# Kernel tuning notes

Hardware: AMD Instinct MI355X
Metric: run time of the kernel (lower is better)

Reference implementation:

```python
import jax, jax.numpy as jnp
import numpy as np

NUM_CH = 4
N_NODES = 20000
N_EDGES = 320000
HEADS = 4
HID = 32
NEG_SLOPE = 0.2


def _edge_type_meta(num_ch):
    # order: spatial (ch->ch) then inter-channel (src!=dst), matching __init__
    src_t = list(range(num_ch)) + [s for s in range(num_ch) for d in range(num_ch) if s != d]
    dst_t = list(range(num_ch)) + [d for s in range(num_ch) for d in range(num_ch) if s != d]
    return src_t, dst_t


def gat_conv(x_src, x_dst, edge_index, W, a_src, a_dst, b):
    """PyG GATConv, concat=False, add_self_loops=False. x_src:[Ns,Fin], W:[Fin,H*C]."""
    H, C = a_src.shape
    n_dst = x_dst.shape[0]
    h_src = (x_src @ W).reshape(-1, H, C)           # [Ns,H,C]
    h_dst = (x_dst @ W).reshape(-1, H, C)           # [Nd,H,C] (shared lin)
    s_score = jnp.sum(h_src * a_src, axis=-1)       # [Ns,H]
    d_score = jnp.sum(h_dst * a_dst, axis=-1)       # [Nd,H]
    src, dst = edge_index[0], edge_index[1]
    e = jax.nn.leaky_relu(s_score[src] + d_score[dst], NEG_SLOPE)  # [E,H]
    # segment softmax over incoming edges of each destination node
    emax = jnp.full((n_dst, H), -jnp.inf, e.dtype).at[dst].max(e)
    p = jnp.exp(e - emax[dst])
    denom = jnp.zeros((n_dst, H), e.dtype).at[dst].add(p)
    alpha = p / denom[dst]                          # [E,H]
    msg = h_src[src] * alpha[:, :, None]            # [E,H,C]
    out = jnp.zeros((n_dst, H, C), msg.dtype).at[dst].add(msg)
    return out.mean(axis=1) + b                     # concat=False -> head mean, + bias


def hetero_layer(x_list, edges, src_t, dst_t, W, a_s, a_d, b):
    num_ch = len(x_list)
    sums = [None] * num_ch
    counts = [0] * num_ch
    for t in range(edges.shape[0]):
        o = gat_conv(x_list[src_t[t]], x_list[dst_t[t]], edges[t], W[t], a_s[t], a_d[t], b[t])
        c = dst_t[t]
        sums[c] = o if sums[c] is None else sums[c] + o
        counts[c] += 1
    return [s / cnt for s, cnt in zip(sums, counts)]  # HeteroConv aggr='mean'


def setup_inputs() -> dict:
    key = jax.random.key(0)
    ks = jax.random.split(key, 10)
    T = NUM_CH + NUM_CH * (NUM_CH - 1)
    scale = 0.1
    return {
        "x": jax.random.normal(ks[0], (NUM_CH, N_NODES, 1), jnp.float32),
        "edges": jax.random.randint(ks[1], (T, 2, N_EDGES), 0, N_NODES, jnp.int32),
        "W1": scale * jax.random.normal(ks[2], (T, 1, HEADS * HID), jnp.float32),
        "att_src1": scale * jax.random.normal(ks[3], (T, HEADS, HID), jnp.float32),
        "att_dst1": scale * jax.random.normal(ks[4], (T, HEADS, HID), jnp.float32),
        "b1": scale * jax.random.normal(ks[5], (T, HID), jnp.float32),
        "W2": scale * jax.random.normal(ks[6], (T, HID, HEADS * HID), jnp.float32),
        "att_src2": scale * jax.random.normal(ks[7], (T, HEADS, HID), jnp.float32),
        "att_dst2": scale * jax.random.normal(ks[8], (T, HEADS, HID), jnp.float32),
        "b2": scale * jax.random.normal(ks[9], (T, HID), jnp.float32),
    }


def reference(x, edges, W1, att_src1, att_dst1, b1, W2, att_src2, att_dst2, b2):
    num_ch = x.shape[0]
    src_t, dst_t = _edge_type_meta(num_ch)
    x_list = [x[c] for c in range(num_ch)]
    h = hetero_layer(x_list, edges, src_t, dst_t, W1, att_src1, att_dst1, b1)
    h = [jax.nn.relu(v) for v in h]  # dropout is identity at inference
    h = hetero_layer(h, edges, src_t, dst_t, W2, att_src2, att_dst2, b2)
    h = [jax.nn.relu(v) for v in h]
    # cat over sorted node-type keys 'ch_0'..'ch_{C-1}' (string sort == numeric for C<=10)
    return jnp.concatenate(h, axis=-1)  # [N, num_ch*HID]
```

## Files before the change

kernel.cpp:

```cpp
#include <hip/hip_runtime.h>
#include <hip/hip_fp16.h>
#include <math.h>

#define NN 20000
#define NE 320000
#define NT 16
#define NEG 0.2f
#define NCHUNK 16
#define CHSZ (NE / NCHUNK)
#define CAP 48

__device__ __forceinline__ int d_src_of(int t) { return t < 4 ? t : (t - 4) / 3; }
__device__ __forceinline__ int d_dst_of(int t) {
    if (t < 4) return t;
    int i = t - 4, s = i / 3, j = i % 3;
    return j + (j >= s ? 1 : 0);
}

__global__ __launch_bounds__(1024) void place3(const int* __restrict__ edges,
                                               unsigned* __restrict__ gcnt,
                                               unsigned short* __restrict__ csr_src) {
    int t = blockIdx.x & 15, chunk = blockIdx.x >> 4;
    __shared__ unsigned h[NN / 2];
    __shared__ unsigned base[NN / 2];
    for (int i = threadIdx.x; i < NN / 2; i += 1024) h[i] = 0;
    __syncthreads();
    const int* srcp = edges + (size_t)t * 2 * NE + chunk * CHSZ;
    const int* dstp = srcp + NE;
    for (int e = threadIdx.x; e < CHSZ; e += 1024) {
        int d = __builtin_nontemporal_load(dstp + e);
        atomicAdd(&h[d >> 1], (d & 1) ? 0x10000u : 1u);
    }
    __syncthreads();
    unsigned* gc = gcnt + (size_t)t * (NN / 2);
    for (int w = threadIdx.x; w < NN / 2; w += 1024) {
        unsigned v = h[w];
        base[w] = v ? atomicAdd(&gc[w], v) : 0u;
        h[w] = 0;
    }
    __syncthreads();
    unsigned short* cs = csr_src + (size_t)t * NN * CAP;
    for (int e = threadIdx.x; e < CHSZ; e += 1024) {
        int d = __builtin_nontemporal_load(dstp + e);
        int sv = __builtin_nontemporal_load(srcp + e);
        unsigned old = atomicAdd(&h[d >> 1], (d & 1) ? 0x10000u : 1u);
        unsigned bs = base[d >> 1];
        int off = (d & 1) ? (int)((old >> 16) + (bs >> 16))
                          : (int)((old & 0xffffu) + (bs & 0xffffu));
        if (off < CAP) cs[(size_t)d * CAP + off] = (unsigned short)sv;
    }
}

__global__ void precompute_u(const float* __restrict__ W1, const float* __restrict__ as1,
                             const float* __restrict__ ad1, const float* __restrict__ W2,
                             const float* __restrict__ as2, const float* __restrict__ ad2,
                             float* __restrict__ u1s, float* __restrict__ u1d,
                             float* __restrict__ u2s, float* __restrict__ u2d) {
    int t = blockIdx.x, tid = threadIdx.x;
    int k = tid >> 2, h = tid & 3;
    float ss = 0.f, dd = 0.f;
    for (int c = 0; c < 32; c++) {
        float w = W2[(size_t)t * 4096 + k * 128 + h * 32 + c];
        ss += w * as2[t * 128 + h * 32 + c];
        dd += w * ad2[t * 128 + h * 32 + c];
    }
    u2s[(t * 32 + k) * 4 + h] = ss;
    u2d[(t * 32 + k) * 4 + h] = dd;
    if (tid < 4) {
        int hh = tid;
        float s1 = 0.f, d1 = 0.f;
        for (int c = 0; c < 32; c++) {
            float w = W1[t * 128 + hh * 32 + c];
            s1 += w * as1[t * 128 + hh * 32 + c];
            d1 += w * ad1[t * 128 + hh * 32 + c];
        }
        u1s[t * 4 + hh] = s1;
        u1d[t * 4 + hh] = d1;
    }
}

__global__ void layer1_fused(const float* __restrict__ x, const unsigned short* __restrict__ csr_src,
                             const unsigned short* __restrict__ cnt16, const float* __restrict__ u1s,
                             const float* __restrict__ u1d, float4* __restrict__ g1) {
    int t = blockIdx.y;
    int d = blockIdx.x * 256 + threadIdx.x;
    if (d >= NN) return;
    int sc = d_src_of(t), dc = d_dst_of(t);
    float xd = x[dc * NN + d];
    float4 usv = ((const float4*)u1s)[t];
    float4 udv = ((const float4*)u1d)[t];
    float us[4] = {usv.x, usv.y, usv.z, usv.w};
    float dl[4] = {xd * udv.x, xd * udv.y, xd * udv.z, xd * udv.w};
    int cnt = cnt16[t * NN + d];
    if (cnt > CAP) cnt = CAP;
    float dn[4] = {0, 0, 0, 0}, a[4] = {0, 0, 0, 0};
    const unsigned short* cs = csr_src + (size_t)t * NN * CAP + (size_t)d * CAP;
#pragma unroll 2
    for (int i = 0; i < cnt; i++) {
        int s = cs[i];
        float xs = x[sc * NN + s];
#pragma unroll
        for (int h = 0; h < 4; h++) {
            float l = xs * us[h] + dl[h];
            l = l > 0.f ? l : NEG * l;
            float p = __expf(l);
            dn[h] += p;
            a[h] += p * xs;
        }
    }
    float4 g;
    g.x = (cnt > 0) ? a[0] / dn[0] : 0.f;
    g.y = (cnt > 0) ? a[1] / dn[1] : 0.f;
    g.z = (cnt > 0) ? a[2] / dn[2] : 0.f;
    g.w = (cnt > 0) ? a[3] / dn[3] : 0.f;
    g1[t * NN + d] = g;
}

__global__ void transform1(const float4* __restrict__ g1, const float* __restrict__ W1,
                           const float* __restrict__ b1, float* __restrict__ x1,
                           __half* __restrict__ x1h) {
    int idx = blockIdx.x * 256 + threadIdx.x;
    if (idx >= 4 * NN * 32) return;
    int c = idx & 31;
    int n = (idx >> 5) % NN;
    int ch = idx / (NN * 32);
    float sum = 0.f, bs = 0.f;
#pragma unroll
    for (int t = 0; t < NT; t++) {
        if (d_dst_of(t) == ch) {
            float4 g = g1[t * NN + n];
            const float* w = W1 + t * 128 + c;
            sum += 0.25f * (g.x * w[0] + g.y * w[32] + g.z * w[64] + g.w * w[96]);
            bs += b1[t * 32 + c];
        }
    }
    float v = 0.25f * (sum + bs);
    v = v > 0.f ? v : 0.f;
    x1[idx] = v;
    x1h[idx] = __float2half(v);
}

__global__ void scores2b(const float* __restrict__ x1, const float* __restrict__ u2s,
                         const float* __restrict__ u2d, float4* __restrict__ ss,
                         float4* __restrict__ ds) {
    int c = blockIdx.y >> 1, half = blockIdx.y & 1;
    int t0 = c, t1, t2, t3;
    if (half == 0) {
        t1 = 4 + c * 3; t2 = t1 + 1; t3 = t1 + 2;
    } else {
        int s1 = (c == 0) ? 1 : 0, s2 = (c <= 1) ? 2 : 1, s3 = (c <= 2) ? 3 : 2;
        t1 = 4 + s1 * 3 + (c > s1 ? c - 1 : c);
        t2 = 4 + s2 * 3 + (c > s2 ? c - 1 : c);
        t3 = 4 + s3 * 3 + (c > s3 ? c - 1 : c);
    }
    __shared__ float4 uS[4][32];
    const float* ub = half ? u2d : u2s;
    if (threadIdx.x < 128) {
        int q = threadIdx.x >> 5, kk = threadIdx.x & 31;
        int tq = (q == 0) ? t0 : (q == 1) ? t1 : (q == 2) ? t2 : t3;
        uS[q][kk] = ((const float4*)(ub + (size_t)tq * 128))[kk];
    }
    __syncthreads();
    int n = blockIdx.x * 256 + threadIdx.x;
    if (n >= NN) return;
    const float4* xr = (const float4*)(x1 + ((size_t)c * NN + n) * 32);
    float4 a0 = {0,0,0,0}, a1 = {0,0,0,0}, a2 = {0,0,0,0}, a3 = {0,0,0,0};
#pragma unroll
    for (int kq = 0; kq < 8; kq++) {
        float4 xv = xr[kq];
#pragma unroll
        for (int m = 0; m < 4; m++) {
            float xk = (&xv.x)[m];
            float4 u0 = uS[0][kq * 4 + m], u1 = uS[1][kq * 4 + m];
            float4 u2v = uS[2][kq * 4 + m], u3 = uS[3][kq * 4 + m];
            a0.x += xk * u0.x; a0.y += xk * u0.y; a0.z += xk * u0.z; a0.w += xk * u0.w;
            a1.x += xk * u1.x; a1.y += xk * u1.y; a1.z += xk * u1.z; a1.w += xk * u1.w;
            a2.x += xk * u2v.x; a2.y += xk * u2v.y; a2.z += xk * u2v.z; a2.w += xk * u2v.w;
            a3.x += xk * u3.x; a3.y += xk * u3.y; a3.z += xk * u3.z; a3.w += xk * u3.w;
        }
    }
    float4* ob = half ? ds : ss;
    ob[(size_t)t0 * NN + n] = a0;
    ob[(size_t)t1 * NN + n] = a1;
    ob[(size_t)t2 * NN + n] = a2;
    ob[(size_t)t3 * NN + n] = a3;
}

__global__ __launch_bounds__(256) void layer2_j(
    const __half* __restrict__ x1h, const unsigned short* __restrict__ csr_src,
    const unsigned short* __restrict__ cnt16, const float4* __restrict__ ss,
    const float4* __restrict__ ds, const float* __restrict__ W2,
    const float* __restrict__ b2, float* __restrict__ out, int j) {
    int b = blockIdx.x;
    int xcd = b & 7;
    int ch = xcd >> 1;
    int dt = (b >> 3) * 2 + (xcd & 1);
    int grp = threadIdx.x >> 5, lane = threadIdx.x & 31;
    int d = dt * 8 + grp;
    __shared__ float4 W2s[1024];
    __shared__ int sStage[8][32];
    __shared__ float4 shbuf4[256];
    float4 (*pStage)[32] = (float4(*)[32])shbuf4;
    float* glu = (float*)shbuf4;
    const float* W2f = (const float*)W2s;
    int gx = (grp & 1) << 2;

    int t, sc;
    if (j == 0) { t = ch; sc = ch; }
    else {
        int s = (j - 1) + ((j - 1) >= ch ? 1 : 0);
        t = 4 + s * 3 + (ch > s ? ch - 1 : ch);
        sc = s;
    }
    const float4* wsrc = (const float4*)(W2 + (size_t)t * 4096);
#pragma unroll
    for (int i = 0; i < 4; i++) W2s[threadIdx.x + i * 256] = wsrc[threadIdx.x + i * 256];
    float4 bq = ((const float4*)(b2 + t * 32))[lane & 7];
    float4 dsv = ds[t * NN + d];
    float dl[4] = {dsv.x, dsv.y, dsv.z, dsv.w};
    int cnt = cnt16[t * NN + d];
    if (cnt > CAP) cnt = CAP;
    float val[4] = {0, 0, 0, 0};
    float dnl[4] = {0, 0, 0, 0};
    const unsigned short* cs = csr_src + (size_t)t * NN * CAP + (size_t)d * CAP;
    const float4* ssb = ss + (size_t)t * NN;
    const __half* xb = x1h + (size_t)sc * NN * 32;
    for (int base = 0; base < cnt; base += 32) {
        int c2 = cnt - base; if (c2 > 32) c2 = 32;
        int myi = base + lane;
        int sIdx = cs[(myi < cnt) ? myi : (cnt - 1)];
        float4 sv = ssb[sIdx];
        float p0, p1, p2, p3;
        { float l = sv.x + dl[0]; l = fmaxf(l, NEG * l); p0 = __expf(l); }
        { float l = sv.y + dl[1]; l = fmaxf(l, NEG * l); p1 = __expf(l); }
        { float l = sv.z + dl[2]; l = fmaxf(l, NEG * l); p2 = __expf(l); }
        { float l = sv.w + dl[3]; l = fmaxf(l, NEG * l); p3 = __expf(l); }
        if (lane >= c2) { p0 = p1 = p2 = p3 = 0.f; }
        dnl[0] += p0; dnl[1] += p1; dnl[2] += p2; dnl[3] += p3;
        sStage[grp][lane] = sIdx;
        pStage[grp][lane] = make_float4(p0, p1, p2, p3);
#pragma unroll 4
        for (int u = 0; u < c2; u++) {
            int s = sStage[grp][u];
            float4 p4 = pStage[grp][u];
            float xk = __half2float(xb[s * 32 + lane]);
            val[0] += p4.x * xk;
            val[1] += p4.y * xk;
            val[2] += p4.z * xk;
            val[3] += p4.w * xk;
        }
    }
#pragma unroll
    for (int off = 1; off <= 16; off <<= 1) {
#pragma unroll
        for (int h = 0; h < 4; h++) dnl[h] += __shfl_xor(dnl[h], off);
    }
    float r0 = (cnt > 0) ? 1.f / dnl[0] : 0.f;
    float r1 = (cnt > 0) ? 1.f / dnl[1] : 0.f;
    float r2 = (cnt > 0) ? 1.f / dnl[2] : 0.f;
    float r3 = (cnt > 0) ? 1.f / dnl[3] : 0.f;
    {
        float* glg = glu + grp * 128;
        glg[      (lane ^ gx)      ] = val[0] * r0;
        glg[ 32 + (lane ^ 8 ^ gx)  ] = val[1] * r1;
        glg[ 64 + (lane ^ 16 ^ gx) ] = val[2] * r2;
        glg[ 96 + (lane ^ 24 ^ gx) ] = val[3] * r3;
    }
    __syncthreads();
    int h = lane >> 3;
    int hmask = (h << 3) ^ gx;
    const float* glh = glu + grp * 128 + h * 32;
    float4 o4 = make_float4(0.f, 0.f, 0.f, 0.f);
#pragma unroll 2
    for (int kq = 0; kq < 8; kq++) {
        float4 g4 = *(const float4*)&glh[(kq * 4) ^ hmask];
        float4 w0 = ((const float4*)(W2f + (kq * 4 + 0) * 128))[lane];
        float4 w1 = ((const float4*)(W2f + (kq * 4 + 1) * 128))[lane];
        float4 w2v = ((const float4*)(W2f + (kq * 4 + 2) * 128))[lane];
        float4 w3 = ((const float4*)(W2f + (kq * 4 + 3) * 128))[lane];
        o4.x += g4.x * w0.x + g4.y * w1.x + g4.z * w2v.x + g4.w * w3.x;
        o4.y += g4.x * w0.y + g4.y * w1.y + g4.z * w2v.y + g4.w * w3.y;
        o4.z += g4.x * w0.z + g4.y * w1.z + g4.z * w2v.z + g4.w * w3.z;
        o4.w += g4.x * w0.w + g4.y * w1.w + g4.z * w2v.w + g4.w * w3.w;
    }
#pragma unroll
    for (int off = 8; off <= 16; off <<= 1) {
        o4.x += __shfl_xor(o4.x, off);
        o4.y += __shfl_xor(o4.y, off);
        o4.z += __shfl_xor(o4.z, off);
        o4.w += __shfl_xor(o4.w, off);
    }
    if (lane < 8) {
        float4 c4;
        c4.x = o4.x * 0.0625f + bq.x * 0.25f;
        c4.y = o4.y * 0.0625f + bq.y * 0.25f;
        c4.z = o4.z * 0.0625f + bq.z * 0.25f;
        c4.w = o4.w * 0.0625f + bq.w * 0.25f;
        float4* oaddr = (float4*)(out + (size_t)d * 128 + ch * 32) + lane;
        if (j > 0) {
            float4 p4 = *oaddr;
            c4.x += p4.x; c4.y += p4.y; c4.z += p4.z; c4.w += p4.w;
        }
        if (j == 3) {
            c4.x = c4.x > 0.f ? c4.x : 0.f;
            c4.y = c4.y > 0.f ? c4.y : 0.f;
            c4.z = c4.z > 0.f ? c4.z : 0.f;
            c4.w = c4.w > 0.f ? c4.w : 0.f;
        }
        *oaddr = c4;
    }
}

extern "C" void kernel_launch(void* const* d_in, const int* in_sizes, int n_in,
                              void* d_out, int out_size, void* d_ws, size_t ws_size,
                              hipStream_t stream) {
    const float* x   = (const float*)d_in[0];
    const int*   edg = (const int*)d_in[1];
    const float* W1  = (const float*)d_in[2];
    const float* as1 = (const float*)d_in[3];
    const float* ad1 = (const float*)d_in[4];
    const float* b1  = (const float*)d_in[5];
    const float* W2  = (const float*)d_in[6];
    const float* as2 = (const float*)d_in[7];
    const float* ad2 = (const float*)d_in[8];
    const float* b2  = (const float*)d_in[9];
    float* out = (float*)d_out;

    char* w = (char*)d_ws;
    auto carve = [&](size_t bytes) {
        void* p = (void*)w;
        w += (bytes + 255) & ~(size_t)255;
        return p;
    };
    unsigned short* csr_src = (unsigned short*)carve((size_t)NT * NN * CAP * 2);
    unsigned*       gcnt    = (unsigned*)carve((size_t)NT * (NN / 2) * 4);
    float* u1s     = (float*)carve(NT * 4 * 4);
    float* u1d     = (float*)carve(NT * 4 * 4);
    float* u2s     = (float*)carve(NT * 32 * 4 * 4);
    float* u2d     = (float*)carve(NT * 32 * 4 * 4);
    float* x1      = (float*)carve((size_t)4 * NN * 32 * 4);
    __half* x1h    = (__half*)carve((size_t)4 * NN * 32 * 2);
    float* ss      = (float*)carve((size_t)NT * NN * 4 * 4);
    float* ds      = (float*)carve((size_t)NT * NN * 4 * 4);
    float4* g1     = (float4*)carve((size_t)NT * NN * 16);
    const unsigned short* cnt16 = (const unsigned short*)gcnt;

    hipMemsetAsync(gcnt, 0, (size_t)NT * (NN / 2) * 4, stream);
    place3<<<NT * NCHUNK, 1024, 0, stream>>>(edg, gcnt, csr_src);
    precompute_u<<<NT, 128, 0, stream>>>(W1, as1, ad1, W2, as2, ad2, u1s, u1d, u2s, u2d);

    dim3 gtn((NN + 255) / 256, NT);
    layer1_fused<<<gtn, 256, 0, stream>>>(x, csr_src, cnt16, u1s, u1d, g1);
    transform1<<<(4 * NN * 32 + 255) / 256, 256, 0, stream>>>(g1, W1, b1, x1, x1h);

    dim3 gs((NN + 255) / 256, 8);
    scores2b<<<gs, 256, 0, stream>>>(x1, u2s, u2d, (float4*)ss, (float4*)ds);
    for (int j = 0; j < 4; j++) {
        layer2_j<<<10000, 256, 0, stream>>>(x1h, csr_src, cnt16, (const float4*)ss,
                                            (const float4*)ds, W2, b2, out, j);
    }
}
```

Measured before the change: 428.5 us.

## Replace shared-memory histogram placement with direct global atomics in edge bucketing

The edge-placement kernel drops the two-pass shared-memory histogram (count, reserve base offsets globally, then place) and instead does one pass where each edge atomically increments the packed global counter and writes its source id into the slot it gets back. The number of chunks per edge type doubles to expose more blocks. This removes one read of the dst array, the LDS init and sync phases, and the per-block base reservation, but turns every edge into a global atomic on contended words. Layer-1 gather loop unroll is also raised from 2 to 4.

New measurement: 544.6 us. +27.1%, slower.

```diff
diff --git a/kernel.cpp b/kernel.cpp
--- a/kernel.cpp
+++ b/kernel.cpp
@@ -6,8 +6,8 @@
 #define NE 320000
 #define NT 16
 #define NEG 0.2f
-#define NCHUNK 16
-#define CHSZ (NE / NCHUNK)
+#define NCHUNK2 32
+#define CHSZ2 (NE / NCHUNK2)
 #define CAP 48
 
 __device__ __forceinline__ int d_src_of(int t) { return t < 4 ? t : (t - 4) / 3; }
@@ -17,36 +17,19 @@
     return j + (j >= s ? 1 : 0);
 }
 
-__global__ __launch_bounds__(1024) void place3(const int* __restrict__ edges,
+__global__ __launch_bounds__(1024) void place4(const int* __restrict__ edges,
                                                unsigned* __restrict__ gcnt,
                                                unsigned short* __restrict__ csr_src) {
     int t = blockIdx.x & 15, chunk = blockIdx.x >> 4;
-    __shared__ unsigned h[NN / 2];
-    __shared__ unsigned base[NN / 2];
-    for (int i = threadIdx.x; i < NN / 2; i += 1024) h[i] = 0;
-    __syncthreads();
-    const int* srcp = edges + (size_t)t * 2 * NE + chunk * CHSZ;
+    const int* srcp = edges + (size_t)t * 2 * NE + chunk * CHSZ2;
     const int* dstp = srcp + NE;
-    for (int e = threadIdx.x; e < CHSZ; e += 1024) {
-        int d = __builtin_nontemporal_load(dstp + e);
-        atomicAdd(&h[d >> 1], (d & 1) ? 0x10000u : 1u);
-    }
-    __syncthreads();
     unsigned* gc = gcnt + (size_t)t * (NN / 2);
-    for (int w = threadIdx.x; w < NN / 2; w += 1024) {
-        unsigned v = h[w];
-        base[w] = v ? atomicAdd(&gc[w], v) : 0u;
-        h[w] = 0;
-    }
-    __syncthreads();
     unsigned short* cs = csr_src + (size_t)t * NN * CAP;
-    for (int e = threadIdx.x; e < CHSZ; e += 1024) {
+    for (int e = threadIdx.x; e < CHSZ2; e += 1024) {
         int d = __builtin_nontemporal_load(dstp + e);
         int sv = __builtin_nontemporal_load(srcp + e);
-        unsigned old = atomicAdd(&h[d >> 1], (d & 1) ? 0x10000u : 1u);
-        unsigned bs = base[d >> 1];
-        int off = (d & 1) ? (int)((old >> 16) + (bs >> 16))
-                          : (int)((old & 0xffffu) + (bs & 0xffffu));
+        unsigned old = atomicAdd(&gc[d >> 1], (d & 1) ? 0x10000u : 1u);
+        int off = (d & 1) ? (int)(old >> 16) : (int)(old & 0xffffu);
         if (off < CAP) cs[(size_t)d * CAP + off] = (unsigned short)sv;
     }
 }
@@ -95,7 +78,7 @@
     if (cnt > CAP) cnt = CAP;
     float dn[4] = {0, 0, 0, 0}, a[4] = {0, 0, 0, 0};
     const unsigned short* cs = csr_src + (size_t)t * NN * CAP + (size_t)d * CAP;
-#pragma unroll 2
+#pragma unroll 4
     for (int i = 0; i < cnt; i++) {
         int s = cs[i];
         float xs = x[sc * NN + s];
@@ -346,7 +329,7 @@
     const unsigned short* cnt16 = (const unsigned short*)gcnt;
 
     hipMemsetAsync(gcnt, 0, (size_t)NT * (NN / 2) * 4, stream);
-    place3<<<NT * NCHUNK, 1024, 0, stream>>>(edg, gcnt, csr_src);
+    place4<<<NT * NCHUNK2, 1024, 0, stream>>>(edg, gcnt, csr_src);
     precompute_u<<<NT, 128, 0, stream>>>(W1, as1, ad1, W2, as2, ad2, u1s, u1d, u2s, u2d);
 
     dim3 gtn((NN + 255) / 256, NT);
```
